# Optimization experiments

Hardware: AMD Instinct MI355X
Metric: run time of the kernel (lower is better)

The kernel has to match this reference:

```python
import jax, jax.numpy as jnp
import numpy as np

RADIUS = 0.3
NEIGHBOR_LIMIT = 32
LN_EPS = 1e-5


def setup_inputs() -> dict:
    key = jax.random.key(0)
    k0, k1, k2 = jax.random.split(key, 3)
    N, C = 16384, 256
    pts = jax.random.normal(k0, (N, 3), jnp.float32)
    masks = jnp.ones((N,), dtype=bool)  # all queries active (fixed shape for jit)
    feats = jax.random.normal(k1, (N, C), jnp.float32)
    W = jax.random.normal(k2, (C, C), jnp.float32) * (1.0 / np.sqrt(C))
    b = jnp.zeros((C,), jnp.float32)
    gamma = jnp.ones((C,), jnp.float32)
    beta = jnp.zeros((C,), jnp.float32)
    return {
        "shifted_src_points_c": pts,
        "src_masks": masks,
        "src_feats_c": feats,
        "W": W,
        "b": b,
        "gamma": gamma,
        "beta": beta,
    }


def _ball_query(q, s, radius, k):
    # squared pairwise distances via the ||q||^2 + ||s||^2 - 2 q.s^T identity
    # (avoids the [N, N, 3] broadcast intermediate)
    q2 = jnp.sum(q * q, axis=-1, keepdims=True)        # [Q, 1]
    s2 = jnp.sum(s * s, axis=-1)                        # [N]
    d2 = q2 + s2[None, :] - 2.0 * (q @ s.T)             # [Q, N]
    neg_d2, idx = jax.lax.top_k(-d2, k)                 # k nearest neighbors
    # out-of-radius slots get index 0, matching the original
    # `neighbor_indices[neighbor_indices == N] = 0` padding replacement
    idx = jnp.where(-neg_d2 > radius * radius, 0, idx)
    return idx                                          # [Q, k] int32


def reference(shifted_src_points_c, src_masks, src_feats_c, W, b, gamma, beta):
    # src_masks is all-True by construction -> queries == all points
    q_nodes = shifted_src_points_c
    idx = _ball_query(q_nodes, shifted_src_points_c, RADIUS, NEIGHBOR_LIMIT)
    group = src_feats_c[idx]                            # [Q, K, C] irregular gather
    pooled = jnp.max(group, axis=1)                     # max over neighbors -> [Q, C]
    h = pooled @ W.T + b                                # nn.Linear(256, 256)
    mu = jnp.mean(h, axis=-1, keepdims=True)
    var = jnp.var(h, axis=-1, keepdims=True)
    h = (h - mu) * jax.lax.rsqrt(var + LN_EPS) * gamma + beta  # LayerNorm
    return jax.nn.relu(h)
```

## Files before the change

kernel.cpp:

```cpp
#include <hip/hip_runtime.h>
#include <stdint.h>

#define NPTS 16384
#define CFEAT 256
#define KNN 32
#define RR_HI 0.0900101f
#define NC 34
#define NCELLS (NC * NC * NC)
#define INVW 3.3332222f
#define NBUCK 128

typedef __attribute__((ext_vector_type(8))) short short8;
typedef __attribute__((ext_vector_type(4))) float floatx4;

__device__ __forceinline__ uint32_t f2bf(uint32_t u) {
  return (u + 0x7fffu + ((u >> 16) & 1u)) >> 16;
}
__device__ __forceinline__ int cell1d(float x) {
  int c = (int)floorf((x + 5.1f) * INVW);
  return min(max(c, 0), NC - 1);
}

__global__ __launch_bounds__(256) void k_prep(const float* __restrict__ feats,
                                              uint16_t* __restrict__ featsb,
                                              const float* __restrict__ Wm,
                                              uint16_t* __restrict__ Wb,
                                              const float* __restrict__ pts,
                                              uint32_t* __restrict__ cellcnt) {
  const int b = blockIdx.x, t = threadIdx.x;
  if (b < 4096) {
    const int i = b * 256 + t;
    const uint4 u = ((const uint4*)feats)[i];
    const uint32_t lo = f2bf(u.x) | (f2bf(u.y) << 16);
    const uint32_t hi = f2bf(u.z) | (f2bf(u.w) << 16);
    ((uint2*)featsb)[i] = make_uint2(lo, hi);
  } else {
    const int i = (b - 4096) * 256 + t;
    const uint4 u = ((const uint4*)Wm)[i];
    const uint32_t lo = f2bf(u.x) | (f2bf(u.y) << 16);
    const uint32_t hi = f2bf(u.z) | (f2bf(u.w) << 16);
    ((uint2*)Wb)[i] = make_uint2(lo, hi);
    const int cx = cell1d(pts[3 * i]), cy = cell1d(pts[3 * i + 1]), cz = cell1d(pts[3 * i + 2]);
    atomicAdd(&cellcnt[(cz * NC + cy) * NC + cx], 1u);
  }
}

__global__ __launch_bounds__(1024) void k_scan(const uint32_t* __restrict__ hist,
                                               uint32_t* __restrict__ start, int n) {
  __shared__ uint32_t wsum[16];
  __shared__ uint32_t carry;
  const int t = threadIdx.x, wv = t >> 6, ln = t & 63;
  if (t == 0) carry = 0;
  __syncthreads();
  const int nq = n >> 2;
  for (int qb = 0; qb < nq; qb += 4096) {
    uint4 v[4];
    uint32_t psum[4];
    uint32_t tot = 0;
    #pragma unroll
    for (int k = 0; k < 4; ++k) {
      const int i4 = qb + t * 4 + k;
      v[k] = (i4 < nq) ? ((const uint4*)hist)[i4] : make_uint4(0, 0, 0, 0);
      psum[k] = tot;
      tot += v[k].x + v[k].y + v[k].z + v[k].w;
    }
    uint32_t s = tot;
    #pragma unroll
    for (int off = 1; off < 64; off <<= 1) {
      uint32_t o = __shfl_up(s, off, 64);
      if (ln >= off) s += o;
    }
    if (ln == 63) wsum[wv] = s;
    const uint32_t cbase = carry;
    __syncthreads();
    uint32_t woff = 0;
    for (int w = 0; w < wv; ++w) woff += wsum[w];
    const uint32_t base = cbase + woff + s - tot;
    #pragma unroll
    for (int k = 0; k < 4; ++k) {
      const int i4 = qb + t * 4 + k;
      if (i4 < nq) {
        const uint32_t e = base + psum[k];
        ((uint4*)start)[i4] =
            make_uint4(e, e + v[k].x, e + v[k].x + v[k].y, e + v[k].x + v[k].y + v[k].z);
      }
    }
    __syncthreads();
    if (t == 1023) carry = base + tot;
    __syncthreads();
  }
  if (t == 0) start[n] = carry;
}

__global__ __launch_bounds__(256) void k_scatter(const float* __restrict__ pts,
                                                 const uint32_t* __restrict__ cellstart,
                                                 uint32_t* __restrict__ cellptr,
                                                 uint32_t* __restrict__ sortedq,
                                                 float4* __restrict__ sortedpts) {
  const int i = blockIdx.x * 256 + threadIdx.x;
  const float x = pts[3 * i], y = pts[3 * i + 1], z = pts[3 * i + 2];
  const int c = (cell1d(z) * NC + cell1d(y)) * NC + cell1d(x);
  const uint32_t pos = cellstart[c] + atomicAdd(&cellptr[c], 1u);
  sortedq[pos] = (uint32_t)i;
  sortedpts[pos] = make_float4(x, y, z, __uint_as_float((uint32_t)i));
}

__global__ __launch_bounds__(256) void k_fsp(const uint32_t* __restrict__ sortedq,
                                             const uint32_t* __restrict__ cellstart,
                                             const float4* __restrict__ sortedpts,
                                             const uint16_t* __restrict__ featsb,
                                             uint16_t* __restrict__ pooledb) {
  __shared__ uint64_t keys[4][256];
  __shared__ uint32_t hist[4][NBUCK];
  __shared__ uint32_t sids[4][KNN];
  const int t = threadIdx.x;
  const int w = t >> 6;
  const int lane = t & 63;
  const uint64_t ltmask = (1ull << lane) - 1ull;
  const int q = (int)sortedq[blockIdx.x * 4 + w];
  const float4 qp = sortedpts[blockIdx.x * 4 + w];
  const float qx = qp.x, qy = qp.y, qz = qp.z;
  const int icx = cell1d(qx), icy = cell1d(qy), icz = cell1d(qz);
  const int x0 = max(icx - 1, 0), x1 = min(icx + 1, NC - 1);
  int S[9], E[9];
  #pragma unroll
  for (int r = 0; r < 9; ++r) {
    const int cz = icz + (r / 3) - 1;
    const int cy = icy + (r % 3) - 1;
    const bool ok = (cz >= 0) && (cz < NC) && (cy >= 0) && (cy < NC);
    const int rb = ((ok ? cz : 0) * NC + (ok ? cy : 0)) * NC;
    const int s = (int)cellstart[rb + x0];
    const int e = (int)cellstart[rb + x1 + 1];
    S[r] = ok ? s : 0;
    E[r] = ok ? e : 0;
  }
  int PRE[10], OFF[9];
  PRE[0] = 0;
  #pragma unroll
  for (int r = 0; r < 9; ++r) {
    PRE[r + 1] = PRE[r] + (E[r] - S[r]);
    OFF[r] = S[r] - PRE[r];
  }
  const int total = PRE[9];
  uint32_t c_run = 0;
  for (int v0 = 0; v0 < total; v0 += 64) {
    const int v = v0 + lane;
    int addr = v + OFF[0];
    #pragma unroll
    for (int r = 1; r < 9; ++r) addr = (v >= PRE[r]) ? (v + OFF[r]) : addr;
    const int ia = min(addr, NPTS - 1);
    const float4 p = sortedpts[ia];
    const float dxf = qx - p.x, dyf = qy - p.y, dzf = qz - p.z;
    const float d2 = __fmaf_rn(dxf, dxf, __fmaf_rn(dyf, dyf, __fmul_rn(dzf, dzf)));
    bool pass = (v < total) && (d2 <= RR_HI);
    uint64_t key = 0;
    if (pass) {
      const double ddx = (double)qx - (double)p.x;
      const double ddy = (double)qy - (double)p.y;
      const double ddz = (double)qz - (double)p.z;
      const double dd2 = fma(ddx, ddx, fma(ddy, ddy, ddz * ddz));
      pass = (dd2 <= 0.3 * 0.3);
      key = ((uint64_t)__double_as_longlong(dd2) & ~0x3FFFull) |
            (uint64_t)__float_as_uint(p.w);
    }
    const uint64_t mask = __ballot(pass);
    if (pass) {
      const uint32_t pos = c_run + (uint32_t)__popcll(mask & ltmask);
      if (pos < 256u) keys[w][pos] = key;
    }
    c_run += (uint32_t)__popcll(mask);
  }
  const int c = (int)min(c_run, 256u);
  if (c <= KNN) {
    if (lane < KNN) sids[w][lane] = (lane < c) ? (uint32_t)(keys[w][lane] & 0x3FFFull) : 0u;
  } else {
    const uint64_t INVALID = ~0ull;
    uint64_t k0 = (lane < c) ? keys[w][lane] : INVALID;
    uint64_t k1 = (lane + 64 < c) ? keys[w][lane + 64] : INVALID;
    uint64_t k2 = (lane + 128 < c) ? keys[w][lane + 128] : INVALID;
    uint64_t k3 = (lane + 192 < c) ? keys[w][lane + 192] : INVALID;
    hist[w][lane] = 0;
    hist[w][lane + 64] = 0;
    int b0 = 999, b1 = 999, b2 = 999, b3 = 999;
    const float bs = 128.0f / 0.09f;
    if (k0 != INVALID) { b0 = min(NBUCK - 1, (int)((float)__longlong_as_double((long long)(k0 & ~0x3FFFull)) * bs)); atomicAdd(&hist[w][b0], 1u); }
    if (k1 != INVALID) { b1 = min(NBUCK - 1, (int)((float)__longlong_as_double((long long)(k1 & ~0x3FFFull)) * bs)); atomicAdd(&hist[w][b1], 1u); }
    if (k2 != INVALID) { b2 = min(NBUCK - 1, (int)((float)__longlong_as_double((long long)(k2 & ~0x3FFFull)) * bs)); atomicAdd(&hist[w][b2], 1u); }
    if (k3 != INVALID) { b3 = min(NBUCK - 1, (int)((float)__longlong_as_double((long long)(k3 & ~0x3FFFull)) * bs)); atomicAdd(&hist[w][b3], 1u); }
    const uint32_t h0 = hist[w][2 * lane], h1 = hist[w][2 * lane + 1];
    const uint32_t tot = h0 + h1;
    uint32_t s = tot;
    #pragma unroll
    for (int off = 1; off < 64; off <<= 1) {
      uint32_t o = __shfl_up(s, off, 64);
      if (lane >= off) s += o;
    }
    const uint32_t C0 = s - tot + h0;
    const uint32_t C1 = s - tot + h0 + h1;
    const uint64_t me = __ballot(C0 >= KNN);
    const uint64_t mo = __ballot(C1 >= KNN);
    const int be = me ? 2 * (__ffsll((unsigned long long)me) - 1) : (1 << 30);
    const int bo = mo ? 2 * (__ffsll((unsigned long long)mo) - 1) + 1 : (1 << 30);
    const int bstar = min(be, bo);
    const uint32_t mval_mine = (bstar & 1) ? (C1 - h1) : (C0 - h0);
    const uint32_t m = (uint32_t)__shfl((int)mval_mine, bstar >> 1, 64);
    uint32_t wpos = 0;
    {
      bool win = (b0 < bstar);
      uint64_t bm = __ballot(win);
      if (win) sids[w][wpos + (uint32_t)__popcll(bm & ltmask)] = (uint32_t)(k0 & 0x3FFFull);
      wpos += (uint32_t)__popcll(bm);
      win = (b1 < bstar); bm = __ballot(win);
      if (win) sids[w][wpos + (uint32_t)__popcll(bm & ltmask)] = (uint32_t)(k1 & 0x3FFFull);
      wpos += (uint32_t)__popcll(bm);
      win = (b2 < bstar); bm = __ballot(win);
      if (win) sids[w][wpos + (uint32_t)__popcll(bm & ltmask)] = (uint32_t)(k2 & 0x3FFFull);
      wpos += (uint32_t)__popcll(bm);
      win = (b3 < bstar); bm = __ballot(win);
      if (win) sids[w][wpos + (uint32_t)__popcll(bm & ltmask)] = (uint32_t)(k3 & 0x3FFFull);
      wpos += (uint32_t)__popcll(bm);
    }
    uint64_t e0 = (b0 == bstar) ? k0 : INVALID;
    uint64_t e1 = (b1 == bstar) ? k1 : INVALID;
    uint64_t e2 = (b2 == bstar) ? k2 : INVALID;
    uint64_t e3 = (b3 == bstar) ? k3 : INVALID;
    const int need = KNN - (int)m;
    for (int it = 0; it < need; ++it) {
      uint64_t a = e0 < e1 ? e0 : e1;
      uint64_t b = e2 < e3 ? e2 : e3;
      uint64_t mn = a < b ? a : b;
      #pragma unroll
      for (int off = 1; off < 64; off <<= 1) {
        uint64_t o = (uint64_t)__shfl_xor((unsigned long long)mn, off, 64);
        mn = o < mn ? o : mn;
      }
      if (e0 == mn) e0 = INVALID;
      else if (e1 == mn) e1 = INVALID;
      else if (e2 == mn) e2 = INVALID;
      else if (e3 == mn) e3 = INVALID;
      if (lane == 0) sids[w][m + it] = (uint32_t)(mn & 0x3FFFull);
    }
  }
  float m0 = -3.0e38f, m1 = -3.0e38f, m2 = -3.0e38f, m3 = -3.0e38f;
  #pragma unroll 8
  for (int k = 0; k < KNN; ++k) {
    const uint32_t idx = sids[w][k];
    const uint2 v = *(const uint2*)(featsb + (size_t)idx * CFEAT + lane * 4);
    m0 = fmaxf(m0, __uint_as_float(v.x << 16));
    m1 = fmaxf(m1, __uint_as_float(v.x & 0xffff0000u));
    m2 = fmaxf(m2, __uint_as_float(v.y << 16));
    m3 = fmaxf(m3, __uint_as_float(v.y & 0xffff0000u));
  }
  const uint32_t lo = (__float_as_uint(m0) >> 16) | (__float_as_uint(m1) & 0xffff0000u);
  const uint32_t hi = (__float_as_uint(m2) >> 16) | (__float_as_uint(m3) & 0xffff0000u);
  ((uint2*)pooledb)[(size_t)q * 64 + lane] = make_uint2(lo, hi);
}

__global__ __launch_bounds__(256) void k_gemm_ln(const uint16_t* __restrict__ pooledb,
                                                 const uint16_t* __restrict__ Wb,
                                                 const float* __restrict__ bias,
                                                 const float* __restrict__ gamma,
                                                 const float* __restrict__ beta,
                                                 float* __restrict__ out) {
  __shared__ uint16_t As[64 * 264];
  __shared__ uint16_t Bs[256 * 40];
  __shared__ float red1[4][64];
  __shared__ float red2[4][64];
  __shared__ float mu_s[64];
  __shared__ float rs_s[64];
  const int t = threadIdx.x;
  const int wave = t >> 6;
  const int lane = t & 63;
  const int quad = lane >> 4;
  const int l15 = lane & 15;
  const int m0 = blockIdx.x * 64;
  {
    const int m = t >> 2, qtr = t & 3;
    const uint4* src = (const uint4*)(pooledb + (size_t)(m0 + m) * 256 + qtr * 64);
    uint4* dst = (uint4*)(As + m * 264 + qtr * 64);
    #pragma unroll
    for (int i = 0; i < 8; ++i) dst[i] = src[i];
  }
  floatx4 acc[4][4];
  #pragma unroll
  for (int mi = 0; mi < 4; ++mi)
    #pragma unroll
    for (int ni = 0; ni < 4; ++ni)
      acc[mi][ni] = (floatx4){0.f, 0.f, 0.f, 0.f};

  for (int step = 0; step < 8; ++step) {
    __syncthreads();
    {
      const uint4* src = (const uint4*)(Wb + (size_t)t * 256 + step * 32);
      uint4* dst = (uint4*)(Bs + t * 40);
      #pragma unroll
      for (int i = 0; i < 4; ++i) dst[i] = src[i];
    }
    __syncthreads();
    short8 a[4], b[4];
    #pragma unroll
    for (int mi = 0; mi < 4; ++mi)
      a[mi] = *(const short8*)(As + (mi * 16 + l15) * 264 + step * 32 + quad * 8);
    #pragma unroll
    for (int ni = 0; ni < 4; ++ni)
      b[ni] = *(const short8*)(Bs + (wave * 64 + ni * 16 + l15) * 40 + quad * 8);
    #pragma unroll
    for (int mi = 0; mi < 4; ++mi)
      #pragma unroll
      for (int ni = 0; ni < 4; ++ni)
        acc[mi][ni] = __builtin_amdgcn_mfma_f32_16x16x32_bf16(a[mi], b[ni], acc[mi][ni], 0, 0, 0);
  }

  float bcol[4], gcol[4], zcol[4];
  #pragma unroll
  for (int ni = 0; ni < 4; ++ni) {
    const int col = wave * 64 + ni * 16 + l15;
    bcol[ni] = bias[col];
    gcol[ni] = gamma[col];
    zcol[ni] = beta[col];
  }
  #pragma unroll
  for (int mi = 0; mi < 4; ++mi)
    #pragma unroll
    for (int ni = 0; ni < 4; ++ni)
      #pragma unroll
      for (int r = 0; r < 4; ++r)
        acc[mi][ni][r] += bcol[ni];
  #pragma unroll
  for (int mi = 0; mi < 4; ++mi) {
    #pragma unroll
    for (int r = 0; r < 4; ++r) {
      const float v0 = acc[mi][0][r], v1 = acc[mi][1][r], v2 = acc[mi][2][r], v3 = acc[mi][3][r];
      float s1 = v0 + v1 + v2 + v3;
      float s2 = v0 * v0 + v1 * v1 + v2 * v2 + v3 * v3;
      #pragma unroll
      for (int off = 1; off < 16; off <<= 1) {
        s1 += __shfl_xor(s1, off, 64);
        s2 += __shfl_xor(s2, off, 64);
      }
      if (l15 == 0) {
        const int row = mi * 16 + quad * 4 + r;
        red1[wave][row] = s1;
        red2[wave][row] = s2;
      }
    }
  }
  __syncthreads();
  if (t < 64) {
    const float s1 = red1[0][t] + red1[1][t] + red1[2][t] + red1[3][t];
    const float s2 = red2[0][t] + red2[1][t] + red2[2][t] + red2[3][t];
    const float mu = s1 * (1.0f / 256.0f);
    const float var = s2 * (1.0f / 256.0f) - mu * mu;
    mu_s[t] = mu;
    rs_s[t] = 1.0f / sqrtf(var + 1e-5f);
  }
  __syncthreads();
  #pragma unroll
  for (int mi = 0; mi < 4; ++mi) {
    #pragma unroll
    for (int r = 0; r < 4; ++r) {
      const int row = mi * 16 + quad * 4 + r;
      const float mu = mu_s[row], rs = rs_s[row];
      #pragma unroll
      for (int ni = 0; ni < 4; ++ni) {
        float y = (acc[mi][ni][r] - mu) * rs * gcol[ni] + zcol[ni];
        out[(size_t)(m0 + row) * 256 + wave * 64 + ni * 16 + l15] = fmaxf(y, 0.0f);
      }
    }
  }
}

extern "C" void kernel_launch(void* const* d_in, const int* in_sizes, int n_in,
                              void* d_out, int out_size, void* d_ws, size_t ws_size,
                              hipStream_t stream) {
  (void)in_sizes; (void)n_in; (void)out_size; (void)ws_size;
  const float* pts   = (const float*)d_in[0];
  const float* feats = (const float*)d_in[2];
  const float* Wm    = (const float*)d_in[3];
  const float* bias  = (const float*)d_in[4];
  const float* gamma = (const float*)d_in[5];
  const float* beta  = (const float*)d_in[6];
  float* out = (float*)d_out;

  uint8_t* ws = (uint8_t*)d_ws;
  uint16_t* featsb    = (uint16_t*)ws;
  uint16_t* Wb        = (uint16_t*)(ws + 8388608);
  uint16_t* pooledb   = (uint16_t*)(ws + 8519680);
  uint32_t* cellcnt   = (uint32_t*)(ws + 16908288);
  uint32_t* cellptr   = (uint32_t*)(ws + 17065728);
  uint32_t* cellstart = (uint32_t*)(ws + 17223168);
  uint32_t* sortedq   = (uint32_t*)(ws + 17380608);
  float4*   sortedpts = (float4*)(ws + 17446144);

  (void)hipMemsetAsync(cellcnt, 0, 2 * 157440, stream);
  k_prep<<<4160, 256, 0, stream>>>(feats, featsb, Wm, Wb, pts, cellcnt);
  k_scan<<<1, 1024, 0, stream>>>(cellcnt, cellstart, NCELLS);
  k_scatter<<<64, 256, 0, stream>>>(pts, cellstart, cellptr, sortedq, sortedpts);
  k_fsp<<<4096, 256, 0, stream>>>(sortedq, cellstart, sortedpts, featsb, pooledb);
  k_gemm_ln<<<256, 256, 0, stream>>>(pooledb, Wb, bias, gamma, beta, out);
}
```

Baseline: 145.8 us.

## Fuse neighbor search/max-pool with GEMM+LayerNorm into one kernel

Merges the ball-query/max-pool kernel and the GEMM+LayerNorm kernel into a single 512-thread block kernel. Each block handles 32 sorted query points, keeps the pooled bf16 rows in shared memory, and then runs the MFMA GEMM and LayerNorm on them, writing results through the sortedq permutation. This removes the pooled intermediate round-trip through global memory and one kernel launch. In exchange, W tiles are reloaded by 512 blocks instead of 256, each wave does four queries serially, and shared memory is aliased between the key buffers and the GEMM tiles.

```diff
diff --git a/kernel.cpp b/kernel.cpp
--- a/kernel.cpp
+++ b/kernel.cpp
@@ -105,250 +105,229 @@
   sortedpts[pos] = make_float4(x, y, z, __uint_as_float((uint32_t)i));
 }
 
-__global__ __launch_bounds__(256) void k_fsp(const uint32_t* __restrict__ sortedq,
-                                             const uint32_t* __restrict__ cellstart,
-                                             const float4* __restrict__ sortedpts,
-                                             const uint16_t* __restrict__ featsb,
-                                             uint16_t* __restrict__ pooledb) {
-  __shared__ uint64_t keys[4][256];
-  __shared__ uint32_t hist[4][NBUCK];
-  __shared__ uint32_t sids[4][KNN];
+__global__ __launch_bounds__(512, 4) void k_fsg(const uint32_t* __restrict__ sortedq,
+                                                const uint32_t* __restrict__ cellstart,
+                                                const float4* __restrict__ sortedpts,
+                                                const uint16_t* __restrict__ featsb,
+                                                const uint16_t* __restrict__ Wb,
+                                                const float* __restrict__ bias,
+                                                const float* __restrict__ gamma,
+                                                const float* __restrict__ beta,
+                                                float* __restrict__ out) {
+  __shared__ __align__(16) uint8_t smem[42752];
   const int t = threadIdx.x;
   const int w = t >> 6;
   const int lane = t & 63;
+  const int quad = lane >> 4;
+  const int l15 = lane & 15;
   const uint64_t ltmask = (1ull << lane) - 1ull;
-  const int q = (int)sortedq[blockIdx.x * 4 + w];
-  const float4 qp = sortedpts[blockIdx.x * 4 + w];
-  const float qx = qp.x, qy = qp.y, qz = qp.z;
-  const int icx = cell1d(qx), icy = cell1d(qy), icz = cell1d(qz);
-  const int x0 = max(icx - 1, 0), x1 = min(icx + 1, NC - 1);
-  int S[9], E[9];
-  #pragma unroll
-  for (int r = 0; r < 9; ++r) {
-    const int cz = icz + (r / 3) - 1;
-    const int cy = icy + (r % 3) - 1;
-    const bool ok = (cz >= 0) && (cz < NC) && (cy >= 0) && (cy < NC);
-    const int rb = ((ok ? cz : 0) * NC + (ok ? cy : 0)) * NC;
-    const int s = (int)cellstart[rb + x0];
-    const int e = (int)cellstart[rb + x1 + 1];
-    S[r] = ok ? s : 0;
-    E[r] = ok ? e : 0;
-  }
-  int PRE[10], OFF[9];
-  PRE[0] = 0;
-  #pragma unroll
-  for (int r = 0; r < 9; ++r) {
-    PRE[r + 1] = PRE[r] + (E[r] - S[r]);
-    OFF[r] = S[r] - PRE[r];
-  }
-  const int total = PRE[9];
-  uint32_t c_run = 0;
-  for (int v0 = 0; v0 < total; v0 += 64) {
-    const int v = v0 + lane;
-    int addr = v + OFF[0];
-    #pragma unroll
-    for (int r = 1; r < 9; ++r) addr = (v >= PRE[r]) ? (v + OFF[r]) : addr;
-    const int ia = min(addr, NPTS - 1);
-    const float4 p = sortedpts[ia];
-    const float dxf = qx - p.x, dyf = qy - p.y, dzf = qz - p.z;
-    const float d2 = __fmaf_rn(dxf, dxf, __fmaf_rn(dyf, dyf, __fmul_rn(dzf, dzf)));
-    bool pass = (v < total) && (d2 <= RR_HI);
-    uint64_t key = 0;
-    if (pass) {
-      const double ddx = (double)qx - (double)p.x;
-      const double ddy = (double)qy - (double)p.y;
-      const double ddz = (double)qz - (double)p.z;
-      const double dd2 = fma(ddx, ddx, fma(ddy, ddy, ddz * ddz));
-      pass = (dd2 <= 0.3 * 0.3);
-      key = ((uint64_t)__double_as_longlong(dd2) & ~0x3FFFull) |
-            (uint64_t)__float_as_uint(p.w);
-    }
-    const uint64_t mask = __ballot(pass);
-    if (pass) {
-      const uint32_t pos = c_run + (uint32_t)__popcll(mask & ltmask);
-      if (pos < 256u) keys[w][pos] = key;
-    }
-    c_run += (uint32_t)__popcll(mask);
-  }
-  const int c = (int)min(c_run, 256u);
-  if (c <= KNN) {
-    if (lane < KNN) sids[w][lane] = (lane < c) ? (uint32_t)(keys[w][lane] & 0x3FFFull) : 0u;
-  } else {
-    const uint64_t INVALID = ~0ull;
-    uint64_t k0 = (lane < c) ? keys[w][lane] : INVALID;
-    uint64_t k1 = (lane + 64 < c) ? keys[w][lane + 64] : INVALID;
-    uint64_t k2 = (lane + 128 < c) ? keys[w][lane + 128] : INVALID;
-    uint64_t k3 = (lane + 192 < c) ? keys[w][lane + 192] : INVALID;
-    hist[w][lane] = 0;
-    hist[w][lane + 64] = 0;
-    int b0 = 999, b1 = 999, b2 = 999, b3 = 999;
-    const float bs = 128.0f / 0.09f;
-    if (k0 != INVALID) { b0 = min(NBUCK - 1, (int)((float)__longlong_as_double((long long)(k0 & ~0x3FFFull)) * bs)); atomicAdd(&hist[w][b0], 1u); }
-    if (k1 != INVALID) { b1 = min(NBUCK - 1, (int)((float)__longlong_as_double((long long)(k1 & ~0x3FFFull)) * bs)); atomicAdd(&hist[w][b1], 1u); }
-    if (k2 != INVALID) { b2 = min(NBUCK - 1, (int)((float)__longlong_as_double((long long)(k2 & ~0x3FFFull)) * bs)); atomicAdd(&hist[w][b2], 1u); }
-    if (k3 != INVALID) { b3 = min(NBUCK - 1, (int)((float)__longlong_as_double((long long)(k3 & ~0x3FFFull)) * bs)); atomicAdd(&hist[w][b3], 1u); }
-    const uint32_t h0 = hist[w][2 * lane], h1 = hist[w][2 * lane + 1];
-    const uint32_t tot = h0 + h1;
-    uint32_t s = tot;
-    #pragma unroll
-    for (int off = 1; off < 64; off <<= 1) {
-      uint32_t o = __shfl_up(s, off, 64);
-      if (lane >= off) s += o;
-    }
-    const uint32_t C0 = s - tot + h0;
-    const uint32_t C1 = s - tot + h0 + h1;
-    const uint64_t me = __ballot(C0 >= KNN);
-    const uint64_t mo = __ballot(C1 >= KNN);
-    const int be = me ? 2 * (__ffsll((unsigned long long)me) - 1) : (1 << 30);
-    const int bo = mo ? 2 * (__ffsll((unsigned long long)mo) - 1) + 1 : (1 << 30);
-    const int bstar = min(be, bo);
-    const uint32_t mval_mine = (bstar & 1) ? (C1 - h1) : (C0 - h0);
-    const uint32_t m = (uint32_t)__shfl((int)mval_mine, bstar >> 1, 64);
-    uint32_t wpos = 0;
-    {
-      bool win = (b0 < bstar);
-      uint64_t bm = __ballot(win);
-      if (win) sids[w][wpos + (uint32_t)__popcll(bm & ltmask)] = (uint32_t)(k0 & 0x3FFFull);
-      wpos += (uint32_t)__popcll(bm);
-      win = (b1 < bstar); bm = __ballot(win);
-      if (win) sids[w][wpos + (uint32_t)__popcll(bm & ltmask)] = (uint32_t)(k1 & 0x3FFFull);
-      wpos += (uint32_t)__popcll(bm);
-      win = (b2 < bstar); bm = __ballot(win);
-      if (win) sids[w][wpos + (uint32_t)__popcll(bm & ltmask)] = (uint32_t)(k2 & 0x3FFFull);
-      wpos += (uint32_t)__popcll(bm);
-      win = (b3 < bstar); bm = __ballot(win);
-      if (win) sids[w][wpos + (uint32_t)__popcll(bm & ltmask)] = (uint32_t)(k3 & 0x3FFFull);
-      wpos += (uint32_t)__popcll(bm);
-    }
-    uint64_t e0 = (b0 == bstar) ? k0 : INVALID;
-    uint64_t e1 = (b1 == bstar) ? k1 : INVALID;
-    uint64_t e2 = (b2 == bstar) ? k2 : INVALID;
-    uint64_t e3 = (b3 == bstar) ? k3 : INVALID;
-    const int need = KNN - (int)m;
-    for (int it = 0; it < need; ++it) {
-      uint64_t a = e0 < e1 ? e0 : e1;
-      uint64_t b = e2 < e3 ? e2 : e3;
-      uint64_t mn = a < b ? a : b;
+  uint64_t* keysw = (uint64_t*)smem + (size_t)w * 256;
+  uint16_t* Bs = (uint16_t*)smem;
+  uint16_t* As = (uint16_t*)(smem + 20480);
+  uint32_t* histw = (uint32_t*)(smem + 37376) + w * NBUCK;
+  float* red1 = (float*)(smem + 37376);
+  float* red2 = red1 + 128;
+  uint32_t* sidsw = (uint32_t*)(smem + 41472) + w * KNN;
+  float* mu_s = (float*)(smem + 42496);
+  float* rs_s = mu_s + 32;
+
+  for (int j = 0; j < 4; ++j) {
+    const int r = w * 4 + j;
+    const int sp = blockIdx.x * 32 + r;
+    const float4 qp = sortedpts[sp];
+    const float qx = qp.x, qy = qp.y, qz = qp.z;
+    const int icx = cell1d(qx), icy = cell1d(qy), icz = cell1d(qz);
+    const int x0 = max(icx - 1, 0), x1 = min(icx + 1, NC - 1);
+    int S[9], E[9];
+    #pragma unroll
+    for (int rr = 0; rr < 9; ++rr) {
+      const int cz = icz + (rr / 3) - 1;
+      const int cy = icy + (rr % 3) - 1;
+      const bool ok = (cz >= 0) && (cz < NC) && (cy >= 0) && (cy < NC);
+      const int rb = ((ok ? cz : 0) * NC + (ok ? cy : 0)) * NC;
+      const int s = (int)cellstart[rb + x0];
+      const int e = (int)cellstart[rb + x1 + 1];
+      S[rr] = ok ? s : 0;
+      E[rr] = ok ? e : 0;
+    }
+    int PRE[10], OFF[9];
+    PRE[0] = 0;
+    #pragma unroll
+    for (int rr = 0; rr < 9; ++rr) {
+      PRE[rr + 1] = PRE[rr] + (E[rr] - S[rr]);
+      OFF[rr] = S[rr] - PRE[rr];
+    }
+    const int total = PRE[9];
+    uint32_t c_run = 0;
+    for (int v0 = 0; v0 < total; v0 += 64) {
+      const int v = v0 + lane;
+      int addr = v + OFF[0];
+      #pragma unroll
+      for (int rr = 1; rr < 9; ++rr) addr = (v >= PRE[rr]) ? (v + OFF[rr]) : addr;
+      const int ia = min(addr, NPTS - 1);
+      const float4 p = sortedpts[ia];
+      const float dxf = qx - p.x, dyf = qy - p.y, dzf = qz - p.z;
+      const float d2 = __fmaf_rn(dxf, dxf, __fmaf_rn(dyf, dyf, __fmul_rn(dzf, dzf)));
+      bool pass = (v < total) && (d2 <= RR_HI);
+      uint64_t key = 0;
+      if (pass) {
+        const double ddx = (double)qx - (double)p.x;
+        const double ddy = (double)qy - (double)p.y;
+        const double ddz = (double)qz - (double)p.z;
+        const double dd2 = fma(ddx, ddx, fma(ddy, ddy, ddz * ddz));
+        pass = (dd2 <= 0.3 * 0.3);
+        key = ((uint64_t)__double_as_longlong(dd2) & ~0x3FFFull) |
+              (uint64_t)__float_as_uint(p.w);
+      }
+      const uint64_t mask = __ballot(pass);
+      if (pass) {
+        const uint32_t pos = c_run + (uint32_t)__popcll(mask & ltmask);
+        if (pos < 256u) keysw[pos] = key;
+      }
+      c_run += (uint32_t)__popcll(mask);
+    }
+    const int c = (int)min(c_run, 256u);
+    if (c <= KNN) {
+      if (lane < KNN) sidsw[lane] = (lane < c) ? (uint32_t)(keysw[lane] & 0x3FFFull) : 0u;
+    } else {
+      const uint64_t INVALID = ~0ull;
+      uint64_t k0 = (lane < c) ? keysw[lane] : INVALID;
+      uint64_t k1 = (lane + 64 < c) ? keysw[lane + 64] : INVALID;
+      uint64_t k2 = (lane + 128 < c) ? keysw[lane + 128] : INVALID;
+      uint64_t k3 = (lane + 192 < c) ? keysw[lane + 192] : INVALID;
+      histw[lane] = 0;
+      histw[lane + 64] = 0;
+      int b0 = 999, b1 = 999, b2 = 999, b3 = 999;
+      const float bs = 128.0f / 0.09f;
+      if (k0 != INVALID) { b0 = min(NBUCK - 1, (int)((float)__longlong_as_double((long long)(k0 & ~0x3FFFull)) * bs)); atomicAdd(&histw[b0], 1u); }
+      if (k1 != INVALID) { b1 = min(NBUCK - 1, (int)((float)__longlong_as_double((long long)(k1 & ~0x3FFFull)) * bs)); atomicAdd(&histw[b1], 1u); }
+      if (k2 != INVALID) { b2 = min(NBUCK - 1, (int)((float)__longlong_as_double((long long)(k2 & ~0x3FFFull)) * bs)); atomicAdd(&histw[b2], 1u); }
+      if (k3 != INVALID) { b3 = min(NBUCK - 1, (int)((float)__longlong_as_double((long long)(k3 & ~0x3FFFull)) * bs)); atomicAdd(&histw[b3], 1u); }
+      const uint32_t h0 = histw[2 * lane], h1 = histw[2 * lane + 1];
+      const uint32_t tot = h0 + h1;
+      uint32_t s = tot;
       #pragma unroll
       for (int off = 1; off < 64; off <<= 1) {
-        uint64_t o = (uint64_t)__shfl_xor((unsigned long long)mn, off, 64);
-        mn = o < mn ? o : mn;
-      }
-      if (e0 == mn) e0 = INVALID;
-      else if (e1 == mn) e1 = INVALID;
-      else if (e2 == mn) e2 = INVALID;
-      else if (e3 == mn) e3 = INVALID;
-      if (lane == 0) sids[w][m + it] = (uint32_t)(mn & 0x3FFFull);
-    }
-  }
-  float m0 = -3.0e38f, m1 = -3.0e38f, m2 = -3.0e38f, m3 = -3.0e38f;
-  #pragma unroll 8
-  for (int k = 0; k < KNN; ++k) {
-    const uint32_t idx = sids[w][k];
-    const uint2 v = *(const uint2*)(featsb + (size_t)idx * CFEAT + lane * 4);
-    m0 = fmaxf(m0, __uint_as_float(v.x << 16));
-    m1 = fmaxf(m1, __uint_as_float(v.x & 0xffff0000u));
-    m2 = fmaxf(m2, __uint_as_float(v.y << 16));
-    m3 = fmaxf(m3, __uint_as_float(v.y & 0xffff0000u));
-  }
-  const uint32_t lo = (__float_as_uint(m0) >> 16) | (__float_as_uint(m1) & 0xffff0000u);
-  const uint32_t hi = (__float_as_uint(m2) >> 16) | (__float_as_uint(m3) & 0xffff0000u);
-  ((uint2*)pooledb)[(size_t)q * 64 + lane] = make_uint2(lo, hi);
-}
-
-__global__ __launch_bounds__(256) void k_gemm_ln(const uint16_t* __restrict__ pooledb,
-                                                 const uint16_t* __restrict__ Wb,
-                                                 const float* __restrict__ bias,
-                                                 const float* __restrict__ gamma,
-                                                 const float* __restrict__ beta,
-                                                 float* __restrict__ out) {
-  __shared__ uint16_t As[64 * 264];
-  __shared__ uint16_t Bs[256 * 40];
-  __shared__ float red1[4][64];
-  __shared__ float red2[4][64];
-  __shared__ float mu_s[64];
-  __shared__ float rs_s[64];
-  const int t = threadIdx.x;
-  const int wave = t >> 6;
-  const int lane = t & 63;
-  const int quad = lane >> 4;
-  const int l15 = lane & 15;
-  const int m0 = blockIdx.x * 64;
-  {
-    const int m = t >> 2, qtr = t & 3;
-    const uint4* src = (const uint4*)(pooledb + (size_t)(m0 + m) * 256 + qtr * 64);
-    uint4* dst = (uint4*)(As + m * 264 + qtr * 64);
-    #pragma unroll
-    for (int i = 0; i < 8; ++i) dst[i] = src[i];
-  }
-  floatx4 acc[4][4];
-  #pragma unroll
-  for (int mi = 0; mi < 4; ++mi)
-    #pragma unroll
-    for (int ni = 0; ni < 4; ++ni)
-      acc[mi][ni] = (floatx4){0.f, 0.f, 0.f, 0.f};
-
+        uint32_t o = __shfl_up(s, off, 64);
+        if (lane >= off) s += o;
+      }
+      const uint32_t C0 = s - tot + h0;
+      const uint32_t C1 = s - tot + h0 + h1;
+      const uint64_t me = __ballot(C0 >= KNN);
+      const uint64_t mo = __ballot(C1 >= KNN);
+      const int be = me ? 2 * (__ffsll((unsigned long long)me) - 1) : (1 << 30);
+      const int bo = mo ? 2 * (__ffsll((unsigned long long)mo) - 1) + 1 : (1 << 30);
+      const int bstar = min(be, bo);
+      const uint32_t mval_mine = (bstar & 1) ? (C1 - h1) : (C0 - h0);
+      const uint32_t m = (uint32_t)__shfl((int)mval_mine, bstar >> 1, 64);
+      uint32_t wpos = 0;
+      {
+        bool win = (b0 < bstar);
+        uint64_t bm = __ballot(win);
+        if (win) sidsw[wpos + (uint32_t)__popcll(bm & ltmask)] = (uint32_t)(k0 & 0x3FFFull);
+        wpos += (uint32_t)__popcll(bm);
+        win = (b1 < bstar); bm = __ballot(win);
+        if (win) sidsw[wpos + (uint32_t)__popcll(bm & ltmask)] = (uint32_t)(k1 & 0x3FFFull);
+        wpos += (uint32_t)__popcll(bm);
+        win = (b2 < bstar); bm = __ballot(win);
+        if (win) sidsw[wpos + (uint32_t)__popcll(bm & ltmask)] = (uint32_t)(k2 & 0x3FFFull);
+        wpos += (uint32_t)__popcll(bm);
+        win = (b3 < bstar); bm = __ballot(win);
+        if (win) sidsw[wpos + (uint32_t)__popcll(bm & ltmask)] = (uint32_t)(k3 & 0x3FFFull);
+        wpos += (uint32_t)__popcll(bm);
+      }
+      uint64_t e0 = (b0 == bstar) ? k0 : INVALID;
+      uint64_t e1 = (b1 == bstar) ? k1 : INVALID;
+      uint64_t e2 = (b2 == bstar) ? k2 : INVALID;
+      uint64_t e3 = (b3 == bstar) ? k3 : INVALID;
+      const int need = KNN - (int)m;
+      for (int it = 0; it < need; ++it) {
+        uint64_t a = e0 < e1 ? e0 : e1;
+        uint64_t b = e2 < e3 ? e2 : e3;
+        uint64_t mn = a < b ? a : b;
+        #pragma unroll
+        for (int off = 1; off < 64; off <<= 1) {
+          uint64_t o = (uint64_t)__shfl_xor((unsigned long long)mn, off, 64);
+          mn = o < mn ? o : mn;
+        }
+        if (e0 == mn) e0 = INVALID;
+        else if (e1 == mn) e1 = INVALID;
+        else if (e2 == mn) e2 = INVALID;
+        else if (e3 == mn) e3 = INVALID;
+        if (lane == 0) sidsw[m + it] = (uint32_t)(mn & 0x3FFFull);
+      }
+    }
+    float m0 = -3.0e38f, m1 = -3.0e38f, m2 = -3.0e38f, m3 = -3.0e38f;
+    #pragma unroll 8
+    for (int k = 0; k < KNN; ++k) {
+      const uint32_t idx = sidsw[k];
+      const uint2 v = *(const uint2*)(featsb + (size_t)idx * CFEAT + lane * 4);
+      m0 = fmaxf(m0, __uint_as_float(v.x << 16));
+      m1 = fmaxf(m1, __uint_as_float(v.x & 0xffff0000u));
+      m2 = fmaxf(m2, __uint_as_float(v.y << 16));
+      m3 = fmaxf(m3, __uint_as_float(v.y & 0xffff0000u));
+    }
+    const uint32_t lo = (__float_as_uint(m0) >> 16) | (__float_as_uint(m1) & 0xffff0000u);
+    const uint32_t hi = (__float_as_uint(m2) >> 16) | (__float_as_uint(m3) & 0xffff0000u);
+    *(uint2*)(As + r * 264 + lane * 4) = make_uint2(lo, hi);
+  }
+
+  const int mt = w >> 2, ns = w & 3;
+  floatx4 acc[4];
+  #pragma unroll
+  for (int nt = 0; nt < 4; ++nt) acc[nt] = (floatx4){0.f, 0.f, 0.f, 0.f};
   for (int step = 0; step < 8; ++step) {
     __syncthreads();
     {
-      const uint4* src = (const uint4*)(Wb + (size_t)t * 256 + step * 32);
-      uint4* dst = (uint4*)(Bs + t * 40);
-      #pragma unroll
-      for (int i = 0; i < 4; ++i) dst[i] = src[i];
-    }
-    __syncthreads();
-    short8 a[4], b[4];
-    #pragma unroll
-    for (int mi = 0; mi < 4; ++mi)
-      a[mi] = *(const short8*)(As + (mi * 16 + l15) * 264 + step * 32 + quad * 8);
-    #pragma unroll
-    for (int ni = 0; ni < 4; ++ni)
-      b[ni] = *(const short8*)(Bs + (wave * 64 + ni * 16 + l15) * 40 + quad * 8);
-    #pragma unroll
-    for (int mi = 0; mi < 4; ++mi)
-      #pragma unroll
-      for (int ni = 0; ni < 4; ++ni)
-        acc[mi][ni] = __builtin_amdgcn_mfma_f32_16x16x32_bf16(a[mi], b[ni], acc[mi][ni], 0, 0, 0);
+      const int row = t >> 1, half = t & 1;
+      const uint4* src = (const uint4*)(Wb + (size_t)row * 256 + step * 32 + half * 16);
+      uint4* dst = (uint4*)(Bs + row * 40 + half * 16);
+      dst[0] = src[0];
+      dst[1] = src[1];
+    }
+    __syncthreads();
+    const short8 a = *(const short8*)(As + (mt * 16 + l15) * 264 + step * 32 + quad * 8);
+    #pragma unroll
+    for (int nt = 0; nt < 4; ++nt) {
+      const short8 b = *(const short8*)(Bs + (ns * 64 + nt * 16 + l15) * 40 + quad * 8);
+      acc[nt] = __builtin_amdgcn_mfma_f32_16x16x32_bf16(a, b, acc[nt], 0, 0, 0);
+    }
   }
 
   float bcol[4], gcol[4], zcol[4];
   #pragma unroll
-  for (int ni = 0; ni < 4; ++ni) {
-    const int col = wave * 64 + ni * 16 + l15;
-    bcol[ni] = bias[col];
-    gcol[ni] = gamma[col];
-    zcol[ni] = beta[col];
-  }
-  #pragma unroll
-  for (int mi = 0; mi < 4; ++mi)
-    #pragma unroll
-    for (int ni = 0; ni < 4; ++ni)
-      #pragma unroll
-      for (int r = 0; r < 4; ++r)
-        acc[mi][ni][r] += bcol[ni];
-  #pragma unroll
-  for (int mi = 0; mi < 4; ++mi) {
-    #pragma unroll
-    for (int r = 0; r < 4; ++r) {
-      const float v0 = acc[mi][0][r], v1 = acc[mi][1][r], v2 = acc[mi][2][r], v3 = acc[mi][3][r];
-      float s1 = v0 + v1 + v2 + v3;
-      float s2 = v0 * v0 + v1 * v1 + v2 * v2 + v3 * v3;
-      #pragma unroll
-      for (int off = 1; off < 16; off <<= 1) {
-        s1 += __shfl_xor(s1, off, 64);
-        s2 += __shfl_xor(s2, off, 64);
-      }
-      if (l15 == 0) {
-        const int row = mi * 16 + quad * 4 + r;
-        red1[wave][row] = s1;
-        red2[wave][row] = s2;
-      }
-    }
-  }
+  for (int nt = 0; nt < 4; ++nt) {
+    const int col = ns * 64 + nt * 16 + l15;
+    bcol[nt] = bias[col];
+    gcol[nt] = gamma[col];
+    zcol[nt] = beta[col];
+  }
+  #pragma unroll
+  for (int nt = 0; nt < 4; ++nt)
+    #pragma unroll
+    for (int rr = 0; rr < 4; ++rr)
+      acc[nt][rr] += bcol[nt];
   __syncthreads();
-  if (t < 64) {
-    const float s1 = red1[0][t] + red1[1][t] + red1[2][t] + red1[3][t];
-    const float s2 = red2[0][t] + red2[1][t] + red2[2][t] + red2[3][t];
+  #pragma unroll
+  for (int rr = 0; rr < 4; ++rr) {
+    const float v0 = acc[0][rr], v1 = acc[1][rr], v2 = acc[2][rr], v3 = acc[3][rr];
+    float s1 = v0 + v1 + v2 + v3;
+    float s2 = v0 * v0 + v1 * v1 + v2 * v2 + v3 * v3;
+    #pragma unroll
+    for (int off = 1; off < 16; off <<= 1) {
+      s1 += __shfl_xor(s1, off, 64);
+      s2 += __shfl_xor(s2, off, 64);
+    }
+    if (l15 == 0) {
+      const int row = mt * 16 + quad * 4 + rr;
+      red1[ns * 32 + row] = s1;
+      red2[ns * 32 + row] = s2;
+    }
+  }
+  __syncthreads();
+  if (t < 32) {
+    const float s1 = red1[t] + red1[32 + t] + red1[64 + t] + red1[96 + t];
+    const float s2 = red2[t] + red2[32 + t] + red2[64 + t] + red2[96 + t];
     const float mu = s1 * (1.0f / 256.0f);
     const float var = s2 * (1.0f / 256.0f) - mu * mu;
     mu_s[t] = mu;
@@ -356,16 +335,14 @@
   }
   __syncthreads();
   #pragma unroll
-  for (int mi = 0; mi < 4; ++mi) {
-    #pragma unroll
-    for (int r = 0; r < 4; ++r) {
-      const int row = mi * 16 + quad * 4 + r;
-      const float mu = mu_s[row], rs = rs_s[row];
-      #pragma unroll
-      for (int ni = 0; ni < 4; ++ni) {
-        float y = (acc[mi][ni][r] - mu) * rs * gcol[ni] + zcol[ni];
-        out[(size_t)(m0 + row) * 256 + wave * 64 + ni * 16 + l15] = fmaxf(y, 0.0f);
-      }
+  for (int rr = 0; rr < 4; ++rr) {
+    const int row = mt * 16 + quad * 4 + rr;
+    const float mu = mu_s[row], rs = rs_s[row];
+    const int q = (int)sortedq[blockIdx.x * 32 + row];
+    #pragma unroll
+    for (int nt = 0; nt < 4; ++nt) {
+      float y = (acc[nt][rr] - mu) * rs * gcol[nt] + zcol[nt];
+      out[(size_t)q * 256 + ns * 64 + nt * 16 + l15] = fmaxf(y, 0.0f);
     }
   }
 }
@@ -385,17 +362,16 @@
   uint8_t* ws = (uint8_t*)d_ws;
   uint16_t* featsb    = (uint16_t*)ws;
   uint16_t* Wb        = (uint16_t*)(ws + 8388608);
-  uint16_t* pooledb   = (uint16_t*)(ws + 8519680);
-  uint32_t* cellcnt   = (uint32_t*)(ws + 16908288);
-  uint32_t* cellptr   = (uint32_t*)(ws + 17065728);
-  uint32_t* cellstart = (uint32_t*)(ws + 17223168);
-  uint32_t* sortedq   = (uint32_t*)(ws + 17380608);
-  float4*   sortedpts = (float4*)(ws + 17446144);
+  uint32_t* cellcnt   = (uint32_t*)(ws + 8519680);
+  uint32_t* cellptr   = (uint32_t*)(ws + 8677120);
+  uint32_t* cellstart = (uint32_t*)(ws + 8834560);
+  uint32_t* sortedq   = (uint32_t*)(ws + 8992000);
+  float4*   sortedpts = (float4*)(ws + 9057536);
 
   (void)hipMemsetAsync(cellcnt, 0, 2 * 157440, stream);
   k_prep<<<4160, 256, 0, stream>>>(feats, featsb, Wm, Wb, pts, cellcnt);
   k_scan<<<1, 1024, 0, stream>>>(cellcnt, cellstart, NCELLS);
   k_scatter<<<64, 256, 0, stream>>>(pts, cellstart, cellptr, sortedq, sortedpts);
-  k_fsp<<<4096, 256, 0, stream>>>(sortedq, cellstart, sortedpts, featsb, pooledb);
-  k_gemm_ln<<<256, 256, 0, stream>>>(pooledb, Wb, bias, gamma, beta, out);
-}
+  k_fsg<<<512, 512, 0, stream>>>(sortedq, cellstart, sortedpts, featsb, Wb,
+                                 bias, gamma, beta, out);
+}
```

After: 152.5 us. 1.05x slower.

## Shrink spatial grid extent and gather neighbor features with 16-byte loads

Applied to the files above, without the earlier changes.

The uniform grid is reduced from 34^3 to 21^3 cells by narrowing the covered coordinate range to about ±3.15. This shrinks the memset, the scan and the cell tables. The max-pool gather now has each half-wave handle alternate neighbors with 128-bit loads, then combines the halves with a cross-lane shuffle. The narrower grid relies on clamping to absorb outlier points beyond ±3.15 into edge cells, which is valid but assumes the Gaussian input rarely lands there.

```diff
diff --git a/kernel.cpp b/kernel.cpp
--- a/kernel.cpp
+++ b/kernel.cpp
@@ -5,8 +5,9 @@
 #define CFEAT 256
 #define KNN 32
 #define RR_HI 0.0900101f
-#define NC 34
+#define NC 21
 #define NCELLS (NC * NC * NC)
+#define NPAD 9264
 #define INVW 3.3332222f
 #define NBUCK 128
 
@@ -17,7 +18,7 @@
   return (u + 0x7fffu + ((u >> 16) & 1u)) >> 16;
 }
 __device__ __forceinline__ int cell1d(float x) {
-  int c = (int)floorf((x + 5.1f) * INVW);
+  int c = (int)floorf((x + 3.15f) * INVW);
   return min(max(c, 0), NC - 1);
 }
 
@@ -242,18 +243,37 @@
     }
   }
   float m0 = -3.0e38f, m1 = -3.0e38f, m2 = -3.0e38f, m3 = -3.0e38f;
-  #pragma unroll 8
-  for (int k = 0; k < KNN; ++k) {
-    const uint32_t idx = sids[w][k];
-    const uint2 v = *(const uint2*)(featsb + (size_t)idx * CFEAT + lane * 4);
+  float m4 = -3.0e38f, m5 = -3.0e38f, m6 = -3.0e38f, m7 = -3.0e38f;
+  const int half = lane >> 5, l31 = lane & 31;
+  #pragma unroll 4
+  for (int k = 0; k < KNN / 2; ++k) {
+    const uint32_t idx = sids[w][2 * k + half];
+    const uint4 v = *(const uint4*)(featsb + (size_t)idx * CFEAT + l31 * 8);
     m0 = fmaxf(m0, __uint_as_float(v.x << 16));
     m1 = fmaxf(m1, __uint_as_float(v.x & 0xffff0000u));
     m2 = fmaxf(m2, __uint_as_float(v.y << 16));
     m3 = fmaxf(m3, __uint_as_float(v.y & 0xffff0000u));
-  }
-  const uint32_t lo = (__float_as_uint(m0) >> 16) | (__float_as_uint(m1) & 0xffff0000u);
-  const uint32_t hi = (__float_as_uint(m2) >> 16) | (__float_as_uint(m3) & 0xffff0000u);
-  ((uint2*)pooledb)[(size_t)q * 64 + lane] = make_uint2(lo, hi);
+    m4 = fmaxf(m4, __uint_as_float(v.z << 16));
+    m5 = fmaxf(m5, __uint_as_float(v.z & 0xffff0000u));
+    m6 = fmaxf(m6, __uint_as_float(v.w << 16));
+    m7 = fmaxf(m7, __uint_as_float(v.w & 0xffff0000u));
+  }
+  m0 = fmaxf(m0, __shfl_xor(m0, 32, 64));
+  m1 = fmaxf(m1, __shfl_xor(m1, 32, 64));
+  m2 = fmaxf(m2, __shfl_xor(m2, 32, 64));
+  m3 = fmaxf(m3, __shfl_xor(m3, 32, 64));
+  m4 = fmaxf(m4, __shfl_xor(m4, 32, 64));
+  m5 = fmaxf(m5, __shfl_xor(m5, 32, 64));
+  m6 = fmaxf(m6, __shfl_xor(m6, 32, 64));
+  m7 = fmaxf(m7, __shfl_xor(m7, 32, 64));
+  if (half == 0) {
+    uint4 o;
+    o.x = (__float_as_uint(m0) >> 16) | (__float_as_uint(m1) & 0xffff0000u);
+    o.y = (__float_as_uint(m2) >> 16) | (__float_as_uint(m3) & 0xffff0000u);
+    o.z = (__float_as_uint(m4) >> 16) | (__float_as_uint(m5) & 0xffff0000u);
+    o.w = (__float_as_uint(m6) >> 16) | (__float_as_uint(m7) & 0xffff0000u);
+    ((uint4*)(pooledb + (size_t)q * CFEAT))[l31] = o;
+  }
 }
 
 __global__ __launch_bounds__(256) void k_gemm_ln(const uint16_t* __restrict__ pooledb,
@@ -387,14 +407,14 @@
   uint16_t* Wb        = (uint16_t*)(ws + 8388608);
   uint16_t* pooledb   = (uint16_t*)(ws + 8519680);
   uint32_t* cellcnt   = (uint32_t*)(ws + 16908288);
-  uint32_t* cellptr   = (uint32_t*)(ws + 17065728);
-  uint32_t* cellstart = (uint32_t*)(ws + 17223168);
-  uint32_t* sortedq   = (uint32_t*)(ws + 17380608);
-  float4*   sortedpts = (float4*)(ws + 17446144);
-
-  (void)hipMemsetAsync(cellcnt, 0, 2 * 157440, stream);
+  uint32_t* cellptr   = (uint32_t*)(ws + 16945408);
+  uint32_t* cellstart = (uint32_t*)(ws + 16982528);
+  uint32_t* sortedq   = (uint32_t*)(ws + 17019648);
+  float4*   sortedpts = (float4*)(ws + 17085184);
+
+  (void)hipMemsetAsync(cellcnt, 0, 2 * 37120, stream);
   k_prep<<<4160, 256, 0, stream>>>(feats, featsb, Wm, Wb, pts, cellcnt);
-  k_scan<<<1, 1024, 0, stream>>>(cellcnt, cellstart, NCELLS);
+  k_scan<<<1, 1024, 0, stream>>>(cellcnt, cellstart, NPAD);
   k_scatter<<<64, 256, 0, stream>>>(pts, cellstart, cellptr, sortedq, sortedpts);
   k_fsp<<<4096, 256, 0, stream>>>(sortedq, cellstart, sortedpts, featsb, pooledb);
   k_gemm_ln<<<256, 256, 0, stream>>>(pooledb, Wb, bias, gamma, beta, out);
```

After: 135.8 us. -6.8%, faster.
